# Kernel tuning notes

Hardware: AMD Instinct MI355X
Metric: run time of the kernel (lower is better)

The kernel has to match this reference:

```python
import jax, jax.numpy as jnp
import numpy as np

BETA = 0.04
EPS_LOW = 0.2
EPS_HIGH = 0.2
TEMPERATURE = 1.0


def setup_inputs() -> dict:
    key = jax.random.key(0)
    ks = jax.random.split(key, 8)
    B, S, H, V = 4, 1024, 2048, 32000
    return {
        "_input": jax.random.normal(ks[0], (B, S, H), dtype=jnp.float32),
        "lin_weight": jax.random.normal(ks[1], (V, H), dtype=jnp.float32) * 0.02,
        "bias": jax.random.normal(ks[2], (V,), dtype=jnp.float32) * 0.02,
        "selected_token_ids": jax.random.randint(ks[3], (B, S), 0, V),
        "attention_mask": jnp.ones((B, S), dtype=jnp.float32),
        "advantages": jax.random.normal(ks[4], (B,), dtype=jnp.float32),
        "ref_per_token_logps": -jnp.abs(jax.random.normal(ks[5], (B, S), dtype=jnp.float32)),
        "old_per_token_logps": -jnp.abs(jax.random.normal(ks[6], (B, S), dtype=jnp.float32)),
    }


def reference(_input, lin_weight, bias, selected_token_ids, attention_mask,
              advantages, ref_per_token_logps, old_per_token_logps):
    B, S, H = _input.shape
    # fused linear projection to vocab logits: [B,S,V]
    logits = (jnp.einsum("bsh,vh->bsv", _input, lin_weight) + bias) / TEMPERATURE
    log_probs = jax.nn.log_softmax(logits, axis=-1)
    per_token_logps = jnp.take_along_axis(
        log_probs, selected_token_ids[..., None], axis=-1)[..., 0]  # [B,S]

    log_ratio = per_token_logps - old_per_token_logps
    seq_len = jnp.clip(attention_mask.sum(-1), 1.0, None)
    seq_level_log_weight = jax.lax.stop_gradient(
        (log_ratio * attention_mask).sum(-1) / seq_len)[:, None]  # [B,1]

    log_importance_weights = (per_token_logps -
                              jax.lax.stop_gradient(per_token_logps) +
                              seq_level_log_weight)
    coef_1 = jnp.exp(log_importance_weights)
    coef_2 = jnp.clip(coef_1, 1.0 - EPS_LOW, 1.0 + EPS_HIGH)
    adv = advantages[:, None]
    per_token_loss = -jnp.minimum(coef_1 * adv, coef_2 * adv)

    # k3 KL penalty (beta != 0, use_ref_model=True)
    d = ref_per_token_logps - per_token_logps
    kl_div = jnp.exp(d) - d - 1.0
    per_token_loss = per_token_loss + BETA * kl_div

    # loss_type == 'grpo'
    loss = ((per_token_loss * attention_mask).sum(-1) / seq_len).sum() / B
    return loss
```

## Files before the change

kernel.cpp:

```cpp
#include <hip/hip_runtime.h>
#include <hip/hip_bf16.h>

#define BETA_C 0.04f
#define EPS_LOW_C 0.2f
#define EPS_HIGH_C 0.2f

static constexpr int B_ = 4, S_ = 1024, H_ = 2048, V_ = 32000;
static constexpr int M_ = B_ * S_;
static constexpr int BM = 256, BN = 256, BK = 64;
static constexpr int NRB = M_ / BM;
static constexpr int NCB = V_ / BN;
static constexpr int NT  = H_ / BK;
static constexpr int NIT = NT / 2;

typedef __attribute__((ext_vector_type(8))) short short8;
typedef __attribute__((ext_vector_type(4))) float f32x4;

__device__ __forceinline__ unsigned short f2bf(float f) {
    unsigned u = __builtin_bit_cast(unsigned, f);
    unsigned r = 0x7FFFu + ((u >> 16) & 1u);
    return (unsigned short)((u + r) >> 16);
}

__device__ __forceinline__ void gload_lds16(const unsigned short* g, unsigned short* l) {
    __builtin_amdgcn_global_load_lds(
        (const __attribute__((address_space(1))) unsigned int*)g,
        (__attribute__((address_space(3))) unsigned int*)l, 16, 0, 0);
}

__global__ void cvt_kernel(const float* __restrict__ in, unsigned short* __restrict__ out, int n4) {
    int i = blockIdx.x * blockDim.x + threadIdx.x;
    int stride = gridDim.x * blockDim.x;
    for (; i < n4; i += stride) {
        float4 v = reinterpret_cast<const float4*>(in)[i];
        ushort4 o;
        o.x = f2bf(v.x); o.y = f2bf(v.y); o.z = f2bf(v.z); o.w = f2bf(v.w);
        reinterpret_cast<ushort4*>(out)[i] = o;
    }
}

__global__ __launch_bounds__(512, 2) void gemm_lse_kernel(
    const unsigned short* __restrict__ A,
    const unsigned short* __restrict__ W,
    const float* __restrict__ bias,
    const int* __restrict__ sel,
    float* __restrict__ partials,
    float* __restrict__ sel_logit)
{
    __shared__ __attribute__((aligned(16))) unsigned short As[2][BM * BK];
    __shared__ __attribute__((aligned(16))) unsigned short Bs[2][BN * BK];
    __shared__ float sums[BM][4];

    const int bid = blockIdx.x;
    const int swz = (bid & 7) * (NRB * NCB / 8) + (bid >> 3);
    const int brow = swz % NRB;
    const int bcol = swz / NRB;
    const int tid  = threadIdx.x;
    const int lane = tid & 63;
    const int wv   = tid >> 6;
    const int wm   = wv >> 2;
    const int wn   = wv & 3;
    const int l15  = lane & 15, lg = lane >> 4;

    int aOff[2][2][4];
    #pragma unroll
    for (int mh = 0; mh < 2; ++mh)
        #pragma unroll
        for (int ks = 0; ks < 2; ++ks)
            #pragma unroll
            for (int mi = 0; mi < 4; ++mi) {
                int row = wm * 128 + (mh * 4 + mi) * 16 + l15;
                aOff[mh][ks][mi] = row * 128 + (((ks * 4 + lg) ^ (row & 7)) << 4);
            }
    int bOff[2][4];
    #pragma unroll
    for (int ks = 0; ks < 2; ++ks)
        #pragma unroll
        for (int n = 0; n < 4; ++n) {
            int row = wn * 64 + n * 16 + l15;
            bOff[ks][n] = row * 128 + (((ks * 4 + lg) ^ (row & 7)) << 4);
        }

    int sLane[2][2];
    #pragma unroll
    for (int i = 0; i < 2; ++i)
        #pragma unroll
        for (int h = 0; h < 2; ++h) {
            int c = i * 512 + tid;
            int r = (c >> 3) + h * 128;
            int gg = (c & 7) ^ (r & 7);
            sLane[i][h] = r * H_ + gg * 8;
        }

    const unsigned short* Ab = A + (long)brow * BM * H_;
    const unsigned short* Wb = W + (long)bcol * BN * H_;

    f32x4 acc[8][4] = {};
    short8 afA[4], afB[4], bfA[4], bfB[4];

#define STG(gb, dst, buf, h, kt) \
    { _Pragma("unroll") \
      for (int i_ = 0; i_ < 2; ++i_) \
          gload_lds16((gb) + sLane[i_][h] + ((kt) & (H_ - 1)), \
                      &dst[buf][(h) * 8192 + (i_ * 512 + tid) * 8]); }

#define RDA(buf, mh, ks, dst) \
    { _Pragma("unroll") \
      for (int mi_ = 0; mi_ < 4; ++mi_) \
          dst[mi_] = *(const short8*)((const char*)&As[0][0] + aOff[mh][ks][mi_] + (buf) * 32768); }

#define RDB(buf, ks, dst) \
    { _Pragma("unroll") \
      for (int n_ = 0; n_ < 4; ++n_) \
          dst[n_] = *(const short8*)((const char*)&Bs[0][0] + bOff[ks][n_] + (buf) * 32768); }

#define MM(mh, afr, bfr) \
    __builtin_amdgcn_s_setprio(1); \
    _Pragma("unroll") \
    for (int mi_ = 0; mi_ < 4; ++mi_) \
    _Pragma("unroll") \
    for (int n_ = 0; n_ < 4; ++n_) \
        acc[(mh) * 4 + mi_][n_] = __builtin_amdgcn_mfma_f32_16x16x32_bf16( \
            afr[mi_], bfr[n_], acc[(mh) * 4 + mi_][n_], 0, 0, 0); \
    __builtin_amdgcn_s_setprio(0);

#define LGKM(n) asm volatile("s_waitcnt lgkmcnt(" #n ")" ::: "memory"); \
    __builtin_amdgcn_sched_barrier(0);
#define VMC(n)  asm volatile("s_waitcnt vmcnt(" #n ")" ::: "memory");
#define BAR     __builtin_amdgcn_s_barrier();
#define SCB     __builtin_amdgcn_sched_barrier(0);

    STG(Ab, As, 0, 0, 0) STG(Ab, As, 0, 1, 0)
    STG(Wb, Bs, 0, 0, 0) STG(Wb, Bs, 0, 1, 0)
    STG(Wb, Bs, 1, 0, 64) STG(Wb, Bs, 1, 1, 64)
    VMC(4)
    BAR
    SCB
    RDA(0, 0, 0, afA) RDB(0, 0, bfA)

    int kA = 64, kB = 128;
    for (int it = 0; it < NIT; ++it) {
        STG(Ab, As, 1, 0, kA)
        BAR
        RDA(0, 1, 0, afB) RDB(0, 1, bfB)
        LGKM(8)
        MM(0, afA, bfA)
        BAR
        STG(Ab, As, 1, 1, kA)
        BAR
        RDA(0, 0, 1, afA)
        LGKM(4)
        MM(1, afB, bfA)
        BAR
        STG(Wb, Bs, 0, 0, kB)
        BAR
        RDA(0, 1, 1, afB)
        LGKM(4)
        MM(0, afA, bfB)
        BAR
        STG(Wb, Bs, 0, 1, kB)
        VMC(4)
        BAR
        SCB
        RDA(1, 0, 0, afA) RDB(1, 0, bfA)
        LGKM(8)
        MM(1, afB, bfB)
        BAR
        STG(Ab, As, 0, 0, kA + 64)
        BAR
        RDA(1, 1, 0, afB) RDB(1, 1, bfB)
        LGKM(8)
        MM(0, afA, bfA)
        BAR
        STG(Ab, As, 0, 1, kA + 64)
        BAR
        RDA(1, 0, 1, afA)
        LGKM(4)
        MM(1, afB, bfA)
        BAR
        STG(Wb, Bs, 1, 0, kB + 64)
        BAR
        RDA(1, 1, 1, afB)
        LGKM(4)
        MM(0, afA, bfB)
        BAR
        STG(Wb, Bs, 1, 1, kB + 64)
        VMC(4)
        BAR
        SCB
        RDA(0, 0, 0, afA) RDB(0, 0, bfA)
        LGKM(8)
        MM(1, afB, bfB)
        BAR

        kA += 128; kB += 128;
    }

    VMC(0)
    asm volatile("s_waitcnt lgkmcnt(0)" ::: "memory");
    __syncthreads();

    const int colb = bcol * BN + wn * 64 + l15;
    float bv[4];
    #pragma unroll
    for (int n = 0; n < 4; ++n) bv[n] = bias[colb + n * 16];

    #pragma unroll
    for (int m = 0; m < 8; ++m) {
        #pragma unroll
        for (int j = 0; j < 4; ++j) {
            const long grow = (long)brow * BM + wm * 128 + m * 16 + lg * 4 + j;
            const int stok = sel[grow];
            float s = 0.f;
            #pragma unroll
            for (int n = 0; n < 4; ++n) {
                float logit = acc[m][n][j] + bv[n];
                s += __expf(logit);
                if (stok == colb + n * 16) sel_logit[grow] = logit;
            }
            s += __shfl_xor(s, 1); s += __shfl_xor(s, 2);
            s += __shfl_xor(s, 4); s += __shfl_xor(s, 8);
            if (l15 == 0) sums[wm * 128 + m * 16 + lg * 4 + j][wn] = s;
        }
    }
    __syncthreads();
    if (tid < BM) {
        float tot = sums[tid][0] + sums[tid][1] + sums[tid][2] + sums[tid][3];
        partials[((long)brow * BM + tid) * NCB + bcol] = tot;
    }
#undef STG
#undef RDA
#undef RDB
#undef MM
#undef LGKM
#undef VMC
#undef BAR
#undef SCB
}

__global__ void reduce_lse_kernel(const float* __restrict__ partials,
                                  const float* __restrict__ sel_logit,
                                  float* __restrict__ lp) {
    const int row = blockIdx.x;
    const int lane = threadIdx.x;
    float s = 0.f;
    for (int i = lane; i < NCB; i += 64) s += partials[(long)row * NCB + i];
    #pragma unroll
    for (int o = 32; o; o >>= 1) s += __shfl_xor(s, o);
    if (lane == 0) lp[row] = sel_logit[row] - __logf(s);
}

__device__ __forceinline__ float block_sum(float v, float* red) {
    const int lane = threadIdx.x & 63, wid = threadIdx.x >> 6;
    #pragma unroll
    for (int o = 32; o; o >>= 1) v += __shfl_xor(v, o);
    if (lane == 0) red[wid] = v;
    __syncthreads();
    if (wid == 0) {
        float x = (lane < 16) ? red[lane] : 0.f;
        #pragma unroll
        for (int o = 8; o; o >>= 1) x += __shfl_xor(x, o);
        if (lane == 0) red[0] = x;
    }
    __syncthreads();
    float r = red[0];
    __syncthreads();
    return r;
}

__global__ __launch_bounds__(1024) void loss_kernel(
    const float* __restrict__ lp, const float* __restrict__ mask,
    const float* __restrict__ adv, const float* __restrict__ ref,
    const float* __restrict__ old, float* __restrict__ out) {
    __shared__ float red[16];
    const int s = threadIdx.x;
    float loss_acc = 0.f;
    for (int b = 0; b < 4; ++b) {
        const int i = b * S_ + s;
        const float mk = mask[i];
        const float lpv = lp[i];
        const float lrsum = block_sum((lpv - old[i]) * mk, red);
        const float msum  = block_sum(mk, red);
        const float seqlen = fmaxf(msum, 1.f);
        const float sw = lrsum / seqlen;
        const float c1 = __expf(sw);
        const float c2 = fminf(fmaxf(c1, 1.f - EPS_LOW_C), 1.f + EPS_HIGH_C);
        const float a = adv[b];
        const float pmin = fminf(c1 * a, c2 * a);
        const float d = ref[i] - lpv;
        const float ptl = -pmin + BETA_C * (__expf(d) - d - 1.f);
        const float lsum = block_sum(ptl * mk, red);
        loss_acc += lsum / seqlen;
    }
    if (s == 0) out[0] = loss_acc * (1.f / (float)B_);
}

extern "C" void kernel_launch(void* const* d_in, const int* in_sizes, int n_in,
                              void* d_out, int out_size, void* d_ws, size_t ws_size,
                              hipStream_t stream) {
    const float* x    = (const float*)d_in[0];
    const float* W    = (const float*)d_in[1];
    const float* bias = (const float*)d_in[2];
    const int*   sel  = (const int*)d_in[3];
    const float* mask = (const float*)d_in[4];
    const float* adv  = (const float*)d_in[5];
    const float* ref  = (const float*)d_in[6];
    const float* old  = (const float*)d_in[7];
    float* out = (float*)d_out;

    char* ws = (char*)d_ws;
    unsigned short* Abf = (unsigned short*)ws;
    unsigned short* Wbf = (unsigned short*)(ws + 16777216);
    float* partials  = (float*)(ws + 16777216 + 131072000);
    float* sel_logit = (float*)(ws + 16777216 + 131072000 + 2048000);
    float* lp        = sel_logit + M_;

    cvt_kernel<<<2048, 256, 0, stream>>>(x, Abf, M_ * H_ / 4);
    cvt_kernel<<<4096, 256, 0, stream>>>(W, Wbf, V_ * H_ / 4);

    gemm_lse_kernel<<<NRB * NCB, 512, 0, stream>>>(Abf, Wbf, bias, sel, partials, sel_logit);

    reduce_lse_kernel<<<M_, 64, 0, stream>>>(partials, sel_logit, lp);
    loss_kernel<<<1, 1024, 0, stream>>>(lp, mask, adv, ref, old, out);
}
```

Before: 654.9 us.

## Restructure GEMM main loop with triple-buffered W tiles in unified LDS

Replaces the separate double-buffered A/B shared arrays with one 160KB LDS region, giving W three rotating buffers and A two. The main loop now processes one k-tile per iteration in four quarter steps, each loading a 2x2 A fragment set and reusing a full B fragment set across both k-substeps. The intent is to prefetch W further ahead and simplify the schedule. In exchange it waits for all LDS reads to finish (lgkmcnt 0) before each MFMA group, which may reduce overlap, and it raises LDS use to the per-CU limit.

```diff
diff --git a/kernel.cpp b/kernel.cpp
--- a/kernel.cpp
+++ b/kernel.cpp
@@ -11,7 +11,6 @@
 static constexpr int NRB = M_ / BM;
 static constexpr int NCB = V_ / BN;
 static constexpr int NT  = H_ / BK;
-static constexpr int NIT = NT / 2;
 
 typedef __attribute__((ext_vector_type(8))) short short8;
 typedef __attribute__((ext_vector_type(4))) float f32x4;
@@ -47,9 +46,7 @@
     float* __restrict__ partials,
     float* __restrict__ sel_logit)
 {
-    __shared__ __attribute__((aligned(16))) unsigned short As[2][BM * BK];
-    __shared__ __attribute__((aligned(16))) unsigned short Bs[2][BN * BK];
-    __shared__ float sums[BM][4];
+    __shared__ __attribute__((aligned(128))) char lds[163840];
 
     const int bid = blockIdx.x;
     const int swz = (bid & 7) * (NRB * NCB / 8) + (bid >> 3);
@@ -62,23 +59,21 @@
     const int wn   = wv & 3;
     const int l15  = lane & 15, lg = lane >> 4;
 
-    int aOff[2][2][4];
-    #pragma unroll
-    for (int mh = 0; mh < 2; ++mh)
-        #pragma unroll
-        for (int ks = 0; ks < 2; ++ks)
-            #pragma unroll
-            for (int mi = 0; mi < 4; ++mi) {
-                int row = wm * 128 + (mh * 4 + mi) * 16 + l15;
-                aOff[mh][ks][mi] = row * 128 + (((ks * 4 + lg) ^ (row & 7)) << 4);
-            }
-    int bOff[2][4];
-    #pragma unroll
-    for (int ks = 0; ks < 2; ++ks)
-        #pragma unroll
-        for (int n = 0; n < 4; ++n) {
+    int aOff[8][2];
+    #pragma unroll
+    for (int m8 = 0; m8 < 8; ++m8)
+        #pragma unroll
+        for (int ks = 0; ks < 2; ++ks) {
+            int row = wm * 128 + m8 * 16 + l15;
+            aOff[m8][ks] = row * 128 + (((ks * 4 + lg) ^ (row & 7)) << 4);
+        }
+    int bOff[4][2];
+    #pragma unroll
+    for (int n = 0; n < 4; ++n)
+        #pragma unroll
+        for (int ks = 0; ks < 2; ++ks) {
             int row = wn * 64 + n * 16 + l15;
-            bOff[ks][n] = row * 128 + (((ks * 4 + lg) ^ (row & 7)) << 4);
+            bOff[n][ks] = row * 128 + (((ks * 4 + lg) ^ (row & 7)) << 4);
         }
 
     int sLane[2][2];
@@ -96,110 +91,93 @@
     const unsigned short* Wb = W + (long)bcol * BN * H_;
 
     f32x4 acc[8][4] = {};
-    short8 afA[4], afB[4], bfA[4], bfB[4];
-
-#define STG(gb, dst, buf, h, kt) \
+    short8 af[2][2], bfr[4][2];
+
+#define STG(gb, bufoff, h, kt) \
     { _Pragma("unroll") \
       for (int i_ = 0; i_ < 2; ++i_) \
           gload_lds16((gb) + sLane[i_][h] + ((kt) & (H_ - 1)), \
-                      &dst[buf][(h) * 8192 + (i_ * 512 + tid) * 8]); }
-
-#define RDA(buf, mh, ks, dst) \
+                      (unsigned short*)(lds + (bufoff) + (h) * 16384 + (i_ * 512 + tid) * 16)); }
+
+#define RDA(abase, q) \
     { _Pragma("unroll") \
-      for (int mi_ = 0; mi_ < 4; ++mi_) \
-          dst[mi_] = *(const short8*)((const char*)&As[0][0] + aOff[mh][ks][mi_] + (buf) * 32768); }
-
-#define RDB(buf, ks, dst) \
+      for (int mi_ = 0; mi_ < 2; ++mi_) \
+      _Pragma("unroll") \
+      for (int ks_ = 0; ks_ < 2; ++ks_) \
+          af[mi_][ks_] = *(const short8*)(lds + (abase) + aOff[(q) * 2 + mi_][ks_]); }
+
+#define RDB(bbase) \
     { _Pragma("unroll") \
       for (int n_ = 0; n_ < 4; ++n_) \
-          dst[n_] = *(const short8*)((const char*)&Bs[0][0] + bOff[ks][n_] + (buf) * 32768); }
-
-#define MM(mh, afr, bfr) \
+      _Pragma("unroll") \
+      for (int ks_ = 0; ks_ < 2; ++ks_) \
+          bfr[n_][ks_] = *(const short8*)(lds + (bbase) + bOff[n_][ks_]); }
+
+#define MM(q) \
     __builtin_amdgcn_s_setprio(1); \
     _Pragma("unroll") \
-    for (int mi_ = 0; mi_ < 4; ++mi_) \
+    for (int ks_ = 0; ks_ < 2; ++ks_) \
+    _Pragma("unroll") \
+    for (int mi_ = 0; mi_ < 2; ++mi_) \
     _Pragma("unroll") \
     for (int n_ = 0; n_ < 4; ++n_) \
-        acc[(mh) * 4 + mi_][n_] = __builtin_amdgcn_mfma_f32_16x16x32_bf16( \
-            afr[mi_], bfr[n_], acc[(mh) * 4 + mi_][n_], 0, 0, 0); \
+        acc[(q) * 2 + mi_][n_] = __builtin_amdgcn_mfma_f32_16x16x32_bf16( \
+            af[mi_][ks_], bfr[n_][ks_], acc[(q) * 2 + mi_][n_], 0, 0, 0); \
     __builtin_amdgcn_s_setprio(0);
 
-#define LGKM(n) asm volatile("s_waitcnt lgkmcnt(" #n ")" ::: "memory"); \
-    __builtin_amdgcn_sched_barrier(0);
+#define LGKM(n) asm volatile("s_waitcnt lgkmcnt(" #n ")" ::: "memory");
 #define VMC(n)  asm volatile("s_waitcnt vmcnt(" #n ")" ::: "memory");
 #define BAR     __builtin_amdgcn_s_barrier();
 #define SCB     __builtin_amdgcn_sched_barrier(0);
 
-    STG(Ab, As, 0, 0, 0) STG(Ab, As, 0, 1, 0)
-    STG(Wb, Bs, 0, 0, 0) STG(Wb, Bs, 0, 1, 0)
-    STG(Wb, Bs, 1, 0, 64) STG(Wb, Bs, 1, 1, 64)
+    STG(Ab, 0, 0, 0)      STG(Ab, 0, 1, 0)
+    STG(Wb, 65536, 0, 0)  STG(Wb, 65536, 1, 0)
+    STG(Wb, 98304, 0, 64) STG(Wb, 98304, 1, 64)
     VMC(4)
     BAR
     SCB
-    RDA(0, 0, 0, afA) RDB(0, 0, bfA)
-
-    int kA = 64, kB = 128;
-    for (int it = 0; it < NIT; ++it) {
-        STG(Ab, As, 1, 0, kA)
-        BAR
-        RDA(0, 1, 0, afB) RDB(0, 1, bfB)
+
+    int aR = 0,     aW = 32768;
+    int bR = 65536, bN = 98304, bW = 131072;
+    int ktA = 64, ktB = 128;
+
+    for (int t = 0; t < NT; ++t) {
+        RDB(bR) RDA(aR, 0)
+        STG(Ab, aW, 0, ktA)
         LGKM(8)
-        MM(0, afA, bfA)
-        BAR
-        STG(Ab, As, 1, 1, kA)
-        BAR
-        RDA(0, 0, 1, afA)
-        LGKM(4)
-        MM(1, afB, bfA)
-        BAR
-        STG(Wb, Bs, 0, 0, kB)
-        BAR
-        RDA(0, 1, 1, afB)
-        LGKM(4)
-        MM(0, afA, bfB)
-        BAR
-        STG(Wb, Bs, 0, 1, kB)
+        BAR
+        LGKM(0) SCB
+        MM(0)
+        BAR
+        RDA(aR, 1)
+        STG(Ab, aW, 1, ktA)
+        BAR
+        LGKM(0) SCB
+        MM(1)
+        BAR
+        RDA(aR, 2)
+        STG(Wb, bW, 0, ktB)
+        BAR
+        LGKM(0) SCB
+        MM(2)
+        BAR
+        RDA(aR, 3)
+        STG(Wb, bW, 1, ktB)
         VMC(4)
         BAR
-        SCB
-        RDA(1, 0, 0, afA) RDB(1, 0, bfA)
-        LGKM(8)
-        MM(1, afB, bfB)
-        BAR
-        STG(Ab, As, 0, 0, kA + 64)
-        BAR
-        RDA(1, 1, 0, afB) RDB(1, 1, bfB)
-        LGKM(8)
-        MM(0, afA, bfA)
-        BAR
-        STG(Ab, As, 0, 1, kA + 64)
-        BAR
-        RDA(1, 0, 1, afA)
-        LGKM(4)
-        MM(1, afB, bfA)
-        BAR
-        STG(Wb, Bs, 1, 0, kB + 64)
-        BAR
-        RDA(1, 1, 1, afB)
-        LGKM(4)
-        MM(0, afA, bfB)
-        BAR
-        STG(Wb, Bs, 1, 1, kB + 64)
-        VMC(4)
-        BAR
-        SCB
-        RDA(0, 0, 0, afA) RDB(0, 0, bfA)
-        LGKM(8)
-        MM(1, afB, bfB)
-        BAR
-
-        kA += 128; kB += 128;
+        LGKM(0) SCB
+        MM(3)
+        BAR
+
+        int ta = aR; aR = aW; aW = ta;
+        int tb = bR; bR = bN; bN = bW; bW = tb;
+        ktA += 64; ktB += 64;
     }
 
     VMC(0)
-    asm volatile("s_waitcnt lgkmcnt(0)" ::: "memory");
-    __syncthreads();
-
+    __syncthreads();
+
+    float* sums = (float*)lds;
     const int colb = bcol * BN + wn * 64 + l15;
     float bv[4];
     #pragma unroll
@@ -220,12 +198,12 @@
             }
             s += __shfl_xor(s, 1); s += __shfl_xor(s, 2);
             s += __shfl_xor(s, 4); s += __shfl_xor(s, 8);
-            if (l15 == 0) sums[wm * 128 + m * 16 + lg * 4 + j][wn] = s;
+            if (l15 == 0) sums[(wm * 128 + m * 16 + lg * 4 + j) * 4 + wn] = s;
         }
     }
     __syncthreads();
     if (tid < BM) {
-        float tot = sums[tid][0] + sums[tid][1] + sums[tid][2] + sums[tid][3];
+        float tot = sums[tid * 4 + 0] + sums[tid * 4 + 1] + sums[tid * 4 + 2] + sums[tid * 4 + 3];
         partials[((long)brow * BM + tid) * NCB + bcol] = tot;
     }
 #undef STG
```

Result: faster. 568.8 us (-13.1%).
